# Kernel optimization log

Hardware: AMD Instinct MI355X
Metric: run time of the kernel (lower is better)

## Reference

```python
import jax, jax.numpy as jnp
import numpy as np

ALPHA = 0.65
KERNEL_RADIUS = 3
BIG = 1e30  # stand-in for +inf in morphological (tropical) convolution


def morphological_kernel(finsler_params, kernel_radius, alpha):
    """Sample the fractional morphological kernel on a (2r+1)x(2r+1) grid.

    F_c(x,y) = sqrt(x^2+y^2) * exp(-sum_k params[c,k] * B_k(theta)) with
    B_1=cos(t), B_2=sin(t), B_3=cos(2t), ... (circular harmonics).
    Kernel for the alpha-homogeneous HJB PDE (t=1):
      k(x) = nu_a * F(x)^(2a/(2a-1)),  nu_a = (2a-1)*(2a)^(-2a/(2a-1)).
    """
    r = kernel_radius
    coords = jnp.arange(-r, r + 1, dtype=finsler_params.dtype)
    yy = coords[:, None]  # [kh,1]
    xx = coords[None, :]  # [1,kw]
    rho = jnp.sqrt(xx * xx + yy * yy)              # [kh,kw]
    theta = jnp.arctan2(yy + 0 * xx, xx + 0 * yy)  # [kh,kw]
    K = finsler_params.shape[1]
    ks = np.arange(1, K + 1)
    freqs = jnp.asarray((ks + 1) // 2, dtype=finsler_params.dtype)  # 1,1,2,2,...
    ang = freqs[:, None, None] * theta[None]                        # [K,kh,kw]
    is_cos = jnp.asarray(ks % 2 == 1)[:, None, None]
    basis = jnp.where(is_cos, jnp.cos(ang), jnp.sin(ang))           # [K,kh,kw]
    F = rho[None] * jnp.exp(-jnp.einsum('ck,kij->cij', finsler_params, basis))  # [C,kh,kw]
    p = 2.0 * alpha / (2.0 * alpha - 1.0)
    nu = (2.0 * alpha - 1.0) * (2.0 * alpha) ** (-p)
    return nu * F ** p  # zero at origin since p>0


def morphological_convolution(u, kernel):
    """out[b,c,y,x] = min_{dy,dx} u[b,c,y+dy,x+dx] + kernel[c,dy+r,dx+r].
    Scan over the (2r+1)^2 stencil offsets with a running min (no huge patches)."""
    B, C, H, W = u.shape
    kh, kw = kernel.shape[1], kernel.shape[2]
    r = kh // 2
    pad = jnp.pad(u, ((0, 0), (0, 0), (r, r), (r, r)), constant_values=BIG)
    kflat = kernel.reshape(C, kh * kw)
    dys, dxs = jnp.meshgrid(jnp.arange(kh), jnp.arange(kw), indexing='ij')
    offs = jnp.stack([dys.reshape(-1), dxs.reshape(-1)], axis=-1)  # [kh*kw,2]

    def step(carry, i):
        dy, dx = offs[i, 0], offs[i, 1]
        sl = jax.lax.dynamic_slice(pad, (0, 0, dy, dx), (B, C, H, W))
        cand = sl + kflat[:, i][None, :, None, None]
        return jnp.minimum(carry, cand), None

    init = jnp.full((B, C, H, W), BIG, u.dtype)
    out, _ = jax.lax.scan(step, init, jnp.arange(kh * kw))
    return out


def convection(u, c):
    """Translation-equivariant transport: out(x) = u(x - c_channel), bilinear
    interpolation, replicate boundary. c[:,0]=x-shift, c[:,1]=y-shift."""
    B, C, H, W = u.shape
    gy = jnp.arange(H, dtype=u.dtype)[None, :, None] - c[:, 1][:, None, None]  # [C,H,1]
    gx = jnp.arange(W, dtype=u.dtype)[None, None, :] - c[:, 0][:, None, None]  # [C,1,W]
    y0 = jnp.floor(gy)
    x0 = jnp.floor(gx)
    wy = gy - y0  # [C,H,1]
    wx = gx - x0  # [C,1,W]
    y0i = jnp.clip(y0.astype(jnp.int32), 0, H - 1)
    y1i = jnp.clip(y0i + 1, 0, H - 1)
    x0i = jnp.clip(x0.astype(jnp.int32), 0, W - 1)
    x1i = jnp.clip(x0i + 1, 0, W - 1)
    ci = jnp.arange(C)[:, None, None]

    def gather(yi, xi):  # yi:[C,H,1], xi:[C,1,W] -> [B,C,H,W]
        return u[:, ci, yi, xi]

    return ((1 - wy) * (1 - wx) * gather(y0i, x0i)
            + (1 - wy) * wx * gather(y0i, x1i)
            + wy * (1 - wx) * gather(y1i, x0i)
            + wy * wx * gather(y1i, x1i))


def cde_pde_layer(x, c, finsler_dil, finsler_ero, weight):
    u = convection(x, c)
    k_dil = morphological_kernel(finsler_dil, KERNEL_RADIUS, ALPHA)
    u = -morphological_convolution(-u, k_dil)           # fractional dilation
    k_ero = morphological_kernel(finsler_ero, KERNEL_RADIUS, ALPHA)
    u = morphological_convolution(u, k_ero)             # fractional erosion
    return jnp.einsum('bihw,io->bohw', u, weight)       # linear channel mix


def setup_inputs() -> dict:
    key = jax.random.key(0)
    k1, k2, k3, k4, k5 = jax.random.split(key, 5)
    B, Cin, Cout, H, W, K = 16, 32, 32, 256, 256, 4
    x = jax.random.normal(k1, (B, Cin, H, W), dtype=jnp.float32)
    c = jax.random.normal(k2, (Cin, 2), dtype=jnp.float32)  # ~kaiming-uniform scale
    finsler_dil = jax.random.uniform(k3, (Cin, K), minval=-1.0, maxval=1.0, dtype=jnp.float32)
    finsler_ero = jax.random.uniform(k4, (Cin, K), minval=-1.0, maxval=1.0, dtype=jnp.float32)
    weight = jax.random.normal(k5, (Cin, Cout), dtype=jnp.float32) / np.sqrt(Cin)
    return {"x": x, "c": c, "finsler_dil": finsler_dil, "finsler_ero": finsler_ero, "weight": weight}


def reference(x, c, finsler_dil, finsler_ero, weight):
    return cde_pde_layer(x, c, finsler_dil, finsler_ero, weight)
```

## Files before the change

kernel.cpp:

```cpp
#include <hip/hip_runtime.h>
#include <math.h>

#define HH 256
#define WW 256
#define NB 16
#define NC 32
#define RAD 3
#define KWID 7
#define NTAPS 49
#define TILE 64
#define CW 76
#define CH 76
#define DSTR 72
#define BUFSZ (CH * CW + 8)
#define BIGF 1e30f
#define FLT_MAX_C 3.402823466e+38f

__global__ void kgen_kernel(const float* __restrict__ fd,
                            const float* __restrict__ fe,
                            float* __restrict__ kd,
                            float* __restrict__ ke) {
    const int c = blockIdx.x;
    const int t = threadIdx.x;
    if (t >= NTAPS) return;
    const int dy = t / KWID - RAD;
    const int dx = t % KWID - RAD;
    const double rho = sqrt((double)(dx * dx + dy * dy));
    const double th  = atan2((double)dy, (double)dx);
    const double alpha = 0.65;
    const double p  = 2.0 * alpha / (2.0 * alpha - 1.0);
    const double nu = (2.0 * alpha - 1.0) * pow(2.0 * alpha, -p);
    const double b1 = cos(th), b2 = sin(th), b3 = cos(2.0 * th), b4 = sin(2.0 * th);
    double s, F;
    s = (double)fd[c * 4 + 0] * b1 + (double)fd[c * 4 + 1] * b2
      + (double)fd[c * 4 + 2] * b3 + (double)fd[c * 4 + 3] * b4;
    F = rho * exp(-s);
    kd[c * NTAPS + t] = (float)(nu * pow(F, p));
    s = (double)fe[c * 4 + 0] * b1 + (double)fe[c * 4 + 1] * b2
      + (double)fe[c * 4 + 2] * b3 + (double)fe[c * 4 + 3] * b4;
    F = rho * exp(-s);
    ke[c * NTAPS + t] = (float)(nu * pow(F, p));
}

__global__ __launch_bounds__(256, 6) void cde_stencil_kernel(
    const float* __restrict__ xin, const float* __restrict__ csh,
    const float* __restrict__ kdil, const float* __restrict__ kero,
    float* __restrict__ uout)
{
    __shared__ float buf[BUFSZ];

    const int tid = threadIdx.x;
    const int tileId = blockIdx.x;
    const int c = blockIdx.y;
    const int b = blockIdx.z;
    const int ty0 = (tileId >> 2) * TILE;
    const int tx0 = (tileId & 3) * TILE;

    const float cx = csh[c * 2 + 0];
    const float cy = csh[c * 2 + 1];
    const float* __restrict__ xb = xin + (((size_t)b * NC + c) << 16);

    const float mcx = -cx, mcy = -cy;
    const float fx0 = floorf(mcx), fy0 = floorf(mcy);
    const float wxf = mcx - fx0, wyf = mcy - fy0;
    const int IX = (int)fx0, IY = (int)fy0;
    const float w00 = (1.f - wyf) * (1.f - wxf);
    const float w01 = (1.f - wyf) * wxf;
    const float w10 = wyf * (1.f - wxf);
    const float w11 = wyf * wxf;

    for (int idx = tid; idx < CH * CW; idx += 256) {
        const int row = idx / CW;
        const int col = idx - row * CW;
        const int gy = ty0 - 6 + row;
        const int gx = tx0 - 6 + col;
        float v = -BIGF;
        if (gy >= 0 && gy < HH && gx >= 0 && gx < WW) {
            const int y0 = min(max(gy + IY, 0), HH - 1);
            const int y1 = min(y0 + 1, HH - 1);
            const int x0 = min(max(gx + IX, 0), WW - 1);
            const int x1 = min(x0 + 1, WW - 1);
            const float a00 = xb[(y0 << 8) + x0];
            const float a01 = xb[(y0 << 8) + x1];
            const float a10 = xb[(y1 << 8) + x0];
            const float a11 = xb[(y1 << 8) + x1];
            v = w00 * a00 + w01 * a01 + w10 * a10 + w11 * a11;
        }
        buf[idx] = v;
    }
    __syncthreads();

    float acc2[5][4];
    int dc0 = 0, dr0 = 0;
    const bool act2 = (tid < 252);
    const float* __restrict__ kdc = kdil + c * NTAPS;
    if (act2) {
        dc0 = (tid % 18) * 4;
        dr0 = (tid / 18) * 5;

        #pragma unroll
        for (int i = 0; i < 5; ++i)
            #pragma unroll
            for (int j = 0; j < 4; ++j) acc2[i][j] = -FLT_MAX_C;

        {
            float ta[28];
            #pragma unroll
            for (int t = 0; t < 28; ++t) ta[t] = kdc[t];
            #pragma unroll
            for (int rr = 0; rr < 8; ++rr) {
                const float* rp = &buf[(dr0 + rr) * CW + dc0];
                const float4 L0 = *reinterpret_cast<const float4*>(rp);
                const float4 L1 = *reinterpret_cast<const float4*>(rp + 4);
                const float4 L2 = *reinterpret_cast<const float4*>(rp + 8);
                const float ld[12] = {L0.x, L0.y, L0.z, L0.w,
                                      L1.x, L1.y, L1.z, L1.w,
                                      L2.x, L2.y, L2.z, L2.w};
                #pragma unroll
                for (int i = 0; i < 5; ++i) {
                    const int ky = rr - i;
                    if (ky < 0 || ky > 3) continue;
                    const int kb = ky * KWID;
                    #pragma unroll
                    for (int j = 0; j < 4; ++j) {
                        float m = acc2[i][j];
                        m = fmaxf(m, fmaxf(ld[j + 0] - ta[kb + 0], ld[j + 1] - ta[kb + 1]));
                        m = fmaxf(m, fmaxf(ld[j + 2] - ta[kb + 2], ld[j + 3] - ta[kb + 3]));
                        m = fmaxf(m, fmaxf(ld[j + 4] - ta[kb + 4], ld[j + 5] - ta[kb + 5]));
                        m = fmaxf(m, ld[j + 6] - ta[kb + 6]);
                        acc2[i][j] = m;
                    }
                }
            }
        }
        {
            float tb[21];
            #pragma unroll
            for (int t = 0; t < 21; ++t) tb[t] = kdc[28 + t];
            #pragma unroll
            for (int rr = 4; rr < 11; ++rr) {
                const float* rp = &buf[(dr0 + rr) * CW + dc0];
                const float4 L0 = *reinterpret_cast<const float4*>(rp);
                const float4 L1 = *reinterpret_cast<const float4*>(rp + 4);
                const float4 L2 = *reinterpret_cast<const float4*>(rp + 8);
                const float ld[12] = {L0.x, L0.y, L0.z, L0.w,
                                      L1.x, L1.y, L1.z, L1.w,
                                      L2.x, L2.y, L2.z, L2.w};
                #pragma unroll
                for (int i = 0; i < 5; ++i) {
                    const int ky = rr - i;
                    if (ky < 4 || ky > 6) continue;
                    const int kb = (ky - 4) * KWID;
                    #pragma unroll
                    for (int j = 0; j < 4; ++j) {
                        float m = acc2[i][j];
                        m = fmaxf(m, fmaxf(ld[j + 0] - tb[kb + 0], ld[j + 1] - tb[kb + 1]));
                        m = fmaxf(m, fmaxf(ld[j + 2] - tb[kb + 2], ld[j + 3] - tb[kb + 3]));
                        m = fmaxf(m, fmaxf(ld[j + 4] - tb[kb + 4], ld[j + 5] - tb[kb + 5]));
                        m = fmaxf(m, ld[j + 6] - tb[kb + 6]);
                        acc2[i][j] = m;
                    }
                }
            }
        }
    }
    __syncthreads();

    if (act2) {
        #pragma unroll
        for (int i = 0; i < 5; ++i) {
            const int dr = dr0 + i;
            const int gy = ty0 - 3 + dr;
            const bool rOK = (gy >= 0) && (gy < HH);
            const int gxb = tx0 - 3 + dc0;
            float4 st;
            st.x = (rOK && (gxb + 0) >= 0 && (gxb + 0) < WW) ? acc2[i][0] : BIGF;
            st.y = (rOK && (gxb + 1) >= 0 && (gxb + 1) < WW) ? acc2[i][1] : BIGF;
            st.z = (rOK && (gxb + 2) >= 0 && (gxb + 2) < WW) ? acc2[i][2] : BIGF;
            st.w = (rOK && (gxb + 3) >= 0 && (gxb + 3) < WW) ? acc2[i][3] : BIGF;
            *reinterpret_cast<float4*>(&buf[dr * DSTR + dc0]) = st;
        }
    }
    __syncthreads();

    {
        const float* __restrict__ kec = kero + c * NTAPS;
        const int ec0 = (tid & 15) * 4;
        const int er0 = (tid >> 4) * 4;

        float acc[4][4];
        #pragma unroll
        for (int i = 0; i < 4; ++i)
            #pragma unroll
            for (int j = 0; j < 4; ++j) acc[i][j] = FLT_MAX_C;

        {
            float ta[28];
            #pragma unroll
            for (int t = 0; t < 28; ++t) ta[t] = kec[t];
            #pragma unroll
            for (int rr = 0; rr < 7; ++rr) {
                const float* rp = &buf[(er0 + rr) * DSTR + ec0];
                const float4 L0 = *reinterpret_cast<const float4*>(rp);
                const float4 L1 = *reinterpret_cast<const float4*>(rp + 4);
                const float4 L2 = *reinterpret_cast<const float4*>(rp + 8);
                const float ld[12] = {L0.x, L0.y, L0.z, L0.w,
                                      L1.x, L1.y, L1.z, L1.w,
                                      L2.x, L2.y, L2.z, L2.w};
                #pragma unroll
                for (int i = 0; i < 4; ++i) {
                    const int ky = rr - i;
                    if (ky < 0 || ky > 3) continue;
                    const int kb = ky * KWID;
                    #pragma unroll
                    for (int j = 0; j < 4; ++j) {
                        float m = acc[i][j];
                        m = fminf(m, fminf(ld[j + 0] + ta[kb + 0], ld[j + 1] + ta[kb + 1]));
                        m = fminf(m, fminf(ld[j + 2] + ta[kb + 2], ld[j + 3] + ta[kb + 3]));
                        m = fminf(m, fminf(ld[j + 4] + ta[kb + 4], ld[j + 5] + ta[kb + 5]));
                        m = fminf(m, ld[j + 6] + ta[kb + 6]);
                        acc[i][j] = m;
                    }
                }
            }
        }
        {
            float tb[21];
            #pragma unroll
            for (int t = 0; t < 21; ++t) tb[t] = kec[28 + t];
            #pragma unroll
            for (int rr = 4; rr < 10; ++rr) {
                const float* rp = &buf[(er0 + rr) * DSTR + ec0];
                const float4 L0 = *reinterpret_cast<const float4*>(rp);
                const float4 L1 = *reinterpret_cast<const float4*>(rp + 4);
                const float4 L2 = *reinterpret_cast<const float4*>(rp + 8);
                const float ld[12] = {L0.x, L0.y, L0.z, L0.w,
                                      L1.x, L1.y, L1.z, L1.w,
                                      L2.x, L2.y, L2.z, L2.w};
                #pragma unroll
                for (int i = 0; i < 4; ++i) {
                    const int ky = rr - i;
                    if (ky < 4 || ky > 6) continue;
                    const int kb = (ky - 4) * KWID;
                    #pragma unroll
                    for (int j = 0; j < 4; ++j) {
                        float m = acc[i][j];
                        m = fminf(m, fminf(ld[j + 0] + tb[kb + 0], ld[j + 1] + tb[kb + 1]));
                        m = fminf(m, fminf(ld[j + 2] + tb[kb + 2], ld[j + 3] + tb[kb + 3]));
                        m = fminf(m, fminf(ld[j + 4] + tb[kb + 4], ld[j + 5] + tb[kb + 5]));
                        m = fminf(m, ld[j + 6] + tb[kb + 6]);
                        acc[i][j] = m;
                    }
                }
            }
        }

        float* __restrict__ ob = uout + (((size_t)b * NC + c) << 16);
        #pragma unroll
        for (int i = 0; i < 4; ++i) {
            float4 st;
            st.x = acc[i][0]; st.y = acc[i][1]; st.z = acc[i][2]; st.w = acc[i][3];
            *reinterpret_cast<float4*>(&ob[((ty0 + er0 + i) << 8) + tx0 + ec0]) = st;
        }
    }
}

__global__ __launch_bounds__(256) void mix_kernel(float* u, const float* __restrict__ wmat) {
    const int p = blockIdx.x * 256 + threadIdx.x;
    const int b = blockIdx.y;
    float* ub = u + ((size_t)b << 21);

    float acc[NC];
    {
        const float v = ub[p];
        #pragma unroll
        for (int o = 0; o < NC; ++o) acc[o] = v * wmat[o];
    }
    #pragma unroll
    for (int i = 1; i < NC; ++i) {
        const float v = ub[(i << 16) + p];
        #pragma unroll
        for (int o = 0; o < NC; ++o)
            acc[o] = fmaf(v, wmat[i * NC + o], acc[o]);
    }
    #pragma unroll
    for (int o = 0; o < NC; ++o) ub[(o << 16) + p] = acc[o];
}

extern "C" void kernel_launch(void* const* d_in, const int* in_sizes, int n_in,
                              void* d_out, int out_size, void* d_ws, size_t ws_size,
                              hipStream_t stream) {
    const float* x  = (const float*)d_in[0];
    const float* c  = (const float*)d_in[1];
    const float* fd = (const float*)d_in[2];
    const float* fe = (const float*)d_in[3];
    const float* w  = (const float*)d_in[4];
    float* out = (float*)d_out;

    float* kd = (float*)d_ws;
    float* ke = kd + NC * NTAPS;

    kgen_kernel<<<dim3(NC), dim3(64), 0, stream>>>(fd, fe, kd, ke);
    cde_stencil_kernel<<<dim3(16, NC, NB), dim3(256), 0, stream>>>(x, c, kd, ke, out);
    mix_kernel<<<dim3((HH * WW) / 256, NB), dim3(256), 0, stream>>>(out, w);
}
```

Baseline: 464.6 us.

## Merge split stencil tap passes, shrink row loads, vectorize channel mix to float2

The dilation and erosion stencils now load all 49 taps into registers at once and run a single pass over the rows, replacing the two half-kernel passes. This drops the re-read of overlapping rows and trims each row load from 12 to 10 floats. The shared-buffer stride for the intermediate becomes CW instead of a separate DSTR, and the halo fill loop updates row/col incrementally instead of dividing each time. The channel-mix kernel processes two pixels per thread with float2 loads and stores and launches half as many blocks. The cost is higher register pressure from 49 taps plus accumulators, and 64 float2 accumulators in mix, which may reduce occupancy.

```diff
diff --git a/kernel.cpp b/kernel.cpp
--- a/kernel.cpp
+++ b/kernel.cpp
@@ -11,7 +11,6 @@
 #define TILE 64
 #define CW 76
 #define CH 76
-#define DSTR 72
 #define BUFSZ (CH * CW + 8)
 #define BIGF 1e30f
 #define FLT_MAX_C 3.402823466e+38f
@@ -69,57 +68,62 @@
     const float w10 = wyf * (1.f - wxf);
     const float w11 = wyf * wxf;
 
-    for (int idx = tid; idx < CH * CW; idx += 256) {
-        const int row = idx / CW;
-        const int col = idx - row * CW;
-        const int gy = ty0 - 6 + row;
-        const int gx = tx0 - 6 + col;
-        float v = -BIGF;
-        if (gy >= 0 && gy < HH && gx >= 0 && gx < WW) {
-            const int y0 = min(max(gy + IY, 0), HH - 1);
-            const int y1 = min(y0 + 1, HH - 1);
-            const int x0 = min(max(gx + IX, 0), WW - 1);
-            const int x1 = min(x0 + 1, WW - 1);
-            const float a00 = xb[(y0 << 8) + x0];
-            const float a01 = xb[(y0 << 8) + x1];
-            const float a10 = xb[(y1 << 8) + x0];
-            const float a11 = xb[(y1 << 8) + x1];
-            v = w00 * a00 + w01 * a01 + w10 * a10 + w11 * a11;
-        }
-        buf[idx] = v;
+    {
+        int row = tid / CW;
+        int col = tid - row * CW;
+        for (int idx = tid; idx < CH * CW; idx += 256) {
+            const int gy = ty0 - 6 + row;
+            const int gx = tx0 - 6 + col;
+            float v = -BIGF;
+            if (gy >= 0 && gy < HH && gx >= 0 && gx < WW) {
+                const int y0 = min(max(gy + IY, 0), HH - 1);
+                const int y1 = min(y0 + 1, HH - 1);
+                const int x0 = min(max(gx + IX, 0), WW - 1);
+                const int x1 = min(x0 + 1, WW - 1);
+                const float a00 = xb[(y0 << 8) + x0];
+                const float a01 = xb[(y0 << 8) + x1];
+                const float a10 = xb[(y1 << 8) + x0];
+                const float a11 = xb[(y1 << 8) + x1];
+                v = w00 * a00 + w01 * a01 + w10 * a10 + w11 * a11;
+            }
+            buf[idx] = v;
+            col += 28; row += 3;
+            if (col >= CW) { col -= CW; ++row; }
+        }
     }
     __syncthreads();
 
     float acc2[5][4];
     int dc0 = 0, dr0 = 0;
     const bool act2 = (tid < 252);
-    const float* __restrict__ kdc = kdil + c * NTAPS;
-    if (act2) {
-        dc0 = (tid % 18) * 4;
-        dr0 = (tid / 18) * 5;
-
-        #pragma unroll
-        for (int i = 0; i < 5; ++i)
-            #pragma unroll
-            for (int j = 0; j < 4; ++j) acc2[i][j] = -FLT_MAX_C;
-
-        {
-            float ta[28];
-            #pragma unroll
-            for (int t = 0; t < 28; ++t) ta[t] = kdc[t];
-            #pragma unroll
-            for (int rr = 0; rr < 8; ++rr) {
-                const float* rp = &buf[(dr0 + rr) * CW + dc0];
+    {
+        const float* __restrict__ kdc = kdil + c * NTAPS;
+        float ta[NTAPS];
+        #pragma unroll
+        for (int t = 0; t < NTAPS; ++t) ta[t] = kdc[t];
+
+        if (act2) {
+            dc0 = (tid % 18) * 4;
+            dr0 = (tid / 18) * 5;
+
+            #pragma unroll
+            for (int i = 0; i < 5; ++i)
+                #pragma unroll
+                for (int j = 0; j < 4; ++j) acc2[i][j] = -FLT_MAX_C;
+
+            const int rb = dr0 * CW + dc0;
+            #pragma unroll
+            for (int rr = 0; rr < 11; ++rr) {
+                const float* rp = &buf[rb + rr * CW];
                 const float4 L0 = *reinterpret_cast<const float4*>(rp);
                 const float4 L1 = *reinterpret_cast<const float4*>(rp + 4);
-                const float4 L2 = *reinterpret_cast<const float4*>(rp + 8);
-                const float ld[12] = {L0.x, L0.y, L0.z, L0.w,
-                                      L1.x, L1.y, L1.z, L1.w,
-                                      L2.x, L2.y, L2.z, L2.w};
+                const float2 L2 = *reinterpret_cast<const float2*>(rp + 8);
+                const float ld[10] = {L0.x, L0.y, L0.z, L0.w,
+                                      L1.x, L1.y, L1.z, L1.w, L2.x, L2.y};
                 #pragma unroll
                 for (int i = 0; i < 5; ++i) {
                     const int ky = rr - i;
-                    if (ky < 0 || ky > 3) continue;
+                    if (ky < 0 || ky > 6) continue;
                     const int kb = ky * KWID;
                     #pragma unroll
                     for (int j = 0; j < 4; ++j) {
@@ -133,36 +137,6 @@
                 }
             }
         }
-        {
-            float tb[21];
-            #pragma unroll
-            for (int t = 0; t < 21; ++t) tb[t] = kdc[28 + t];
-            #pragma unroll
-            for (int rr = 4; rr < 11; ++rr) {
-                const float* rp = &buf[(dr0 + rr) * CW + dc0];
-                const float4 L0 = *reinterpret_cast<const float4*>(rp);
-                const float4 L1 = *reinterpret_cast<const float4*>(rp + 4);
-                const float4 L2 = *reinterpret_cast<const float4*>(rp + 8);
-                const float ld[12] = {L0.x, L0.y, L0.z, L0.w,
-                                      L1.x, L1.y, L1.z, L1.w,
-                                      L2.x, L2.y, L2.z, L2.w};
-                #pragma unroll
-                for (int i = 0; i < 5; ++i) {
-                    const int ky = rr - i;
-                    if (ky < 4 || ky > 6) continue;
-                    const int kb = (ky - 4) * KWID;
-                    #pragma unroll
-                    for (int j = 0; j < 4; ++j) {
-                        float m = acc2[i][j];
-                        m = fmaxf(m, fmaxf(ld[j + 0] - tb[kb + 0], ld[j + 1] - tb[kb + 1]));
-                        m = fmaxf(m, fmaxf(ld[j + 2] - tb[kb + 2], ld[j + 3] - tb[kb + 3]));
-                        m = fmaxf(m, fmaxf(ld[j + 4] - tb[kb + 4], ld[j + 5] - tb[kb + 5]));
-                        m = fmaxf(m, ld[j + 6] - tb[kb + 6]);
-                        acc2[i][j] = m;
-                    }
-                }
-            }
-        }
     }
     __syncthreads();
 
@@ -178,13 +152,17 @@
             st.y = (rOK && (gxb + 1) >= 0 && (gxb + 1) < WW) ? acc2[i][1] : BIGF;
             st.z = (rOK && (gxb + 2) >= 0 && (gxb + 2) < WW) ? acc2[i][2] : BIGF;
             st.w = (rOK && (gxb + 3) >= 0 && (gxb + 3) < WW) ? acc2[i][3] : BIGF;
-            *reinterpret_cast<float4*>(&buf[dr * DSTR + dc0]) = st;
+            *reinterpret_cast<float4*>(&buf[dr * CW + dc0]) = st;
         }
     }
     __syncthreads();
 
     {
         const float* __restrict__ kec = kero + c * NTAPS;
+        float te[NTAPS];
+        #pragma unroll
+        for (int t = 0; t < NTAPS; ++t) te[t] = kec[t];
+
         const int ec0 = (tid & 15) * 4;
         const int er0 = (tid >> 4) * 4;
 
@@ -194,63 +172,28 @@
             #pragma unroll
             for (int j = 0; j < 4; ++j) acc[i][j] = FLT_MAX_C;
 
-        {
-            float ta[28];
-            #pragma unroll
-            for (int t = 0; t < 28; ++t) ta[t] = kec[t];
-            #pragma unroll
-            for (int rr = 0; rr < 7; ++rr) {
-                const float* rp = &buf[(er0 + rr) * DSTR + ec0];
-                const float4 L0 = *reinterpret_cast<const float4*>(rp);
-                const float4 L1 = *reinterpret_cast<const float4*>(rp + 4);
-                const float4 L2 = *reinterpret_cast<const float4*>(rp + 8);
-                const float ld[12] = {L0.x, L0.y, L0.z, L0.w,
-                                      L1.x, L1.y, L1.z, L1.w,
-                                      L2.x, L2.y, L2.z, L2.w};
+        const int rb = er0 * CW + ec0;
+        #pragma unroll
+        for (int rr = 0; rr < 10; ++rr) {
+            const float* rp = &buf[rb + rr * CW];
+            const float4 L0 = *reinterpret_cast<const float4*>(rp);
+            const float4 L1 = *reinterpret_cast<const float4*>(rp + 4);
+            const float2 L2 = *reinterpret_cast<const float2*>(rp + 8);
+            const float ld[10] = {L0.x, L0.y, L0.z, L0.w,
+                                  L1.x, L1.y, L1.z, L1.w, L2.x, L2.y};
+            #pragma unroll
+            for (int i = 0; i < 4; ++i) {
+                const int ky = rr - i;
+                if (ky < 0 || ky > 6) continue;
+                const int kb = ky * KWID;
                 #pragma unroll
-                for (int i = 0; i < 4; ++i) {
-                    const int ky = rr - i;
-                    if (ky < 0 || ky > 3) continue;
-                    const int kb = ky * KWID;
-                    #pragma unroll
-                    for (int j = 0; j < 4; ++j) {
-                        float m = acc[i][j];
-                        m = fminf(m, fminf(ld[j + 0] + ta[kb + 0], ld[j + 1] + ta[kb + 1]));
-                        m = fminf(m, fminf(ld[j + 2] + ta[kb + 2], ld[j + 3] + ta[kb + 3]));
-                        m = fminf(m, fminf(ld[j + 4] + ta[kb + 4], ld[j + 5] + ta[kb + 5]));
-                        m = fminf(m, ld[j + 6] + ta[kb + 6]);
-                        acc[i][j] = m;
-                    }
-                }
-            }
-        }
-        {
-            float tb[21];
-            #pragma unroll
-            for (int t = 0; t < 21; ++t) tb[t] = kec[28 + t];
-            #pragma unroll
-            for (int rr = 4; rr < 10; ++rr) {
-                const float* rp = &buf[(er0 + rr) * DSTR + ec0];
-                const float4 L0 = *reinterpret_cast<const float4*>(rp);
-                const float4 L1 = *reinterpret_cast<const float4*>(rp + 4);
-                const float4 L2 = *reinterpret_cast<const float4*>(rp + 8);
-                const float ld[12] = {L0.x, L0.y, L0.z, L0.w,
-                                      L1.x, L1.y, L1.z, L1.w,
-                                      L2.x, L2.y, L2.z, L2.w};
-                #pragma unroll
-                for (int i = 0; i < 4; ++i) {
-                    const int ky = rr - i;
-                    if (ky < 4 || ky > 6) continue;
-                    const int kb = (ky - 4) * KWID;
-                    #pragma unroll
-                    for (int j = 0; j < 4; ++j) {
-                        float m = acc[i][j];
-                        m = fminf(m, fminf(ld[j + 0] + tb[kb + 0], ld[j + 1] + tb[kb + 1]));
-                        m = fminf(m, fminf(ld[j + 2] + tb[kb + 2], ld[j + 3] + tb[kb + 3]));
-                        m = fminf(m, fminf(ld[j + 4] + tb[kb + 4], ld[j + 5] + tb[kb + 5]));
-                        m = fminf(m, ld[j + 6] + tb[kb + 6]);
-                        acc[i][j] = m;
-                    }
+                for (int j = 0; j < 4; ++j) {
+                    float m = acc[i][j];
+                    m = fminf(m, fminf(ld[j + 0] + te[kb + 0], ld[j + 1] + te[kb + 1]));
+                    m = fminf(m, fminf(ld[j + 2] + te[kb + 2], ld[j + 3] + te[kb + 3]));
+                    m = fminf(m, fminf(ld[j + 4] + te[kb + 4], ld[j + 5] + te[kb + 5]));
+                    m = fminf(m, ld[j + 6] + te[kb + 6]);
+                    acc[i][j] = m;
                 }
             }
         }
@@ -268,23 +211,30 @@
 __global__ __launch_bounds__(256) void mix_kernel(float* u, const float* __restrict__ wmat) {
     const int p = blockIdx.x * 256 + threadIdx.x;
     const int b = blockIdx.y;
-    float* ub = u + ((size_t)b << 21);
-
-    float acc[NC];
-    {
-        const float v = ub[p];
-        #pragma unroll
-        for (int o = 0; o < NC; ++o) acc[o] = v * wmat[o];
+    float2* ub = reinterpret_cast<float2*>(u + ((size_t)b << 21));
+
+    float2 acc[NC];
+    {
+        const float2 v = ub[p];
+        #pragma unroll
+        for (int o = 0; o < NC; ++o) {
+            const float w = wmat[o];
+            acc[o].x = v.x * w;
+            acc[o].y = v.y * w;
+        }
     }
     #pragma unroll
     for (int i = 1; i < NC; ++i) {
-        const float v = ub[(i << 16) + p];
-        #pragma unroll
-        for (int o = 0; o < NC; ++o)
-            acc[o] = fmaf(v, wmat[i * NC + o], acc[o]);
+        const float2 v = ub[(i << 15) + p];
+        #pragma unroll
+        for (int o = 0; o < NC; ++o) {
+            const float w = wmat[i * NC + o];
+            acc[o].x = fmaf(v.x, w, acc[o].x);
+            acc[o].y = fmaf(v.y, w, acc[o].y);
+        }
     }
     #pragma unroll
-    for (int o = 0; o < NC; ++o) ub[(o << 16) + p] = acc[o];
+    for (int o = 0; o < NC; ++o) ub[(o << 15) + p] = acc[o];
 }
 
 extern "C" void kernel_launch(void* const* d_in, const int* in_sizes, int n_in,
@@ -302,5 +252,5 @@
 
     kgen_kernel<<<dim3(NC), dim3(64), 0, stream>>>(fd, fe, kd, ke);
     cde_stencil_kernel<<<dim3(16, NC, NB), dim3(256), 0, stream>>>(x, c, kd, ke, out);
-    mix_kernel<<<dim3((HH * WW) / 256, NB), dim3(256), 0, stream>>>(out, w);
-}
+    mix_kernel<<<dim3((HH * WW / 2) / 256, NB), dim3(256), 0, stream>>>(out, w);
+}
```

New measurement: 557.4 us. 1.2x slower.
